# Kernel optimization log

Hardware: AMD Instinct MI355X
Metric: run time of the kernel (lower is better)

Reference implementation:

```python
import jax, jax.numpy as jnp
import numpy as np

KH, KW, STRIDE, PAD, DIL = 3, 3, 1, 1, 1


def setup_inputs() -> dict:
    key = jax.random.key(0)
    ks = jax.random.split(key, 4)
    B, C, H, W, O = 4, 256, 64, 64, 256
    K = KH * KW
    x = jax.random.normal(ks[0], (B, C, H, W), jnp.float32)
    # offset/mask conv params (original inits to zero; use small random so offsets are non-trivial)
    w_om = jax.random.normal(ks[1], (3 * K, C, KH, KW), jnp.float32) * 0.01
    b_om = jnp.zeros((3 * K,), jnp.float32)
    # main weight: kaiming_uniform_(a=1) -> gain = sqrt(2/(1+1^2)) = 1, bound = sqrt(3)/sqrt(fan_in)
    fan_in = C * K
    bound = float(np.sqrt(3.0) / np.sqrt(fan_in))
    weight = jax.random.uniform(ks[2], (O, C, KH, KW), jnp.float32, -bound, bound)
    bias = jnp.zeros((O,), jnp.float32)
    return {"x": x, "w_om": w_om, "b_om": b_om, "weight": weight, "bias": bias}


def _deform_conv2d(x, offset, mask, weight, bias):
    # torchvision.ops.deform_conv2d semantics, deformable_groups=1, stride=1, pad=1, dil=1
    B, C, H, W = x.shape
    K = KH * KW
    # torchvision offset layout: per-tap interleaved (y, x) pairs along channel dim
    off_y = offset[:, 0::2]  # [B, K, H, W]
    off_x = offset[:, 1::2]  # [B, K, H, W]
    ky = (jnp.repeat(jnp.arange(KH), KW) * DIL).astype(x.dtype)  # [K]
    kx = (jnp.tile(jnp.arange(KW), KH) * DIL).astype(x.dtype)    # [K]
    base_y = (jnp.arange(H) * STRIDE - PAD).astype(x.dtype)
    base_x = (jnp.arange(W) * STRIDE - PAD).astype(x.dtype)
    py = base_y[None, None, :, None] + ky[None, :, None, None] + off_y  # [B,K,H,W]
    px = base_x[None, None, None, :] + kx[None, :, None, None] + off_x  # [B,K,H,W]
    y0 = jnp.floor(py)
    x0 = jnp.floor(px)
    ly = py - y0
    lx = px - x0
    y0i = y0.astype(jnp.int32)
    x0i = x0.astype(jnp.int32)
    x_flat = x.reshape(B, C, H * W)

    def gather(yy, xx):
        # zero-padded gather of one bilinear corner -> [B, C, K, H, W]
        valid = ((yy >= 0) & (yy < H) & (xx >= 0) & (xx < W)).astype(x.dtype)
        idx = (jnp.clip(yy, 0, H - 1) * W + jnp.clip(xx, 0, W - 1)).reshape(B, -1)
        g = jax.vmap(lambda xf, i: jnp.take(xf, i, axis=1))(x_flat, idx)
        return g.reshape(B, C, K, H, W) * valid.reshape(B, 1, K, H, W)

    w00 = ((1 - ly) * (1 - lx))[:, None]
    w01 = ((1 - ly) * lx)[:, None]
    w10 = (ly * (1 - lx))[:, None]
    w11 = (ly * lx)[:, None]
    val = (gather(y0i, x0i) * w00 + gather(y0i, x0i + 1) * w01
           + gather(y0i + 1, x0i) * w10 + gather(y0i + 1, x0i + 1) * w11)
    cols = val * mask[:, None]  # modulated columns [B,C,K,H,W]
    out = jnp.einsum('bckhw,ock->bohw', cols, weight.reshape(weight.shape[0], C, K))
    return out + bias[None, :, None, None]


def reference(x, w_om, b_om, weight, bias):
    om = jax.lax.conv_general_dilated(
        x, w_om, (STRIDE, STRIDE), ((PAD, PAD), (PAD, PAD)),
        rhs_dilation=(DIL, DIL), dimension_numbers=('NCHW', 'OIHW', 'NCHW'),
    ) + b_om[None, :, None, None]
    K = KH * KW
    o1, o2, m = om[:, :K], om[:, K:2 * K], om[:, 2 * K:]
    offset = jnp.concatenate([o1, o2], axis=1)  # [B, 2K, H, W]
    mask = jax.nn.sigmoid(m)                    # [B, K, H, W]
    return _deform_conv2d(x, offset, mask, weight, bias)
```

## Files before the change

kernel.cpp:

```cpp
#include <hip/hip_runtime.h>
#include <stdint.h>

#define B_ 4
#define C_ 256
#define H_ 64
#define W_ 64
#define O_ 256
#define K_ 9
#define CK 2304
#define HW 4096
#define NTOT 16384

typedef __bf16 bf16x8 __attribute__((ext_vector_type(8)));
typedef __bf16 bf16x4 __attribute__((ext_vector_type(4)));
typedef float f32x4 __attribute__((ext_vector_type(4)));
typedef float f32x2 __attribute__((ext_vector_type(2)));
typedef f32x2 __attribute__((aligned(4))) f32x2u;

__device__ __forceinline__ uint16_t f2bf(float f) {
  uint32_t u = __builtin_bit_cast(uint32_t, f);
  return (uint16_t)((u + 0x7FFFu + ((u >> 16) & 1u)) >> 16);
}

__device__ __forceinline__ uint32_t pk_bf16(float a, float b) {
  uint16_t lo = __builtin_bit_cast(uint16_t, (__bf16)a);
  uint16_t hi = __builtin_bit_cast(uint16_t, (__bf16)b);
  return (uint32_t)lo | ((uint32_t)hi << 16);
}

__global__ void kA_prep(const float* __restrict__ weight, const float* __restrict__ w_om,
                        const float* __restrict__ x, uint16_t* __restrict__ wb,
                        uint16_t* __restrict__ womb, uint16_t* __restrict__ xT) {
  int bx = blockIdx.x;
  int t = threadIdx.x;
  if (bx < 256) {
    int o = bx, c = t;
    const float* wp = weight + (o * 256 + c) * 9;
#pragma unroll
    for (int k = 0; k < 9; ++k) wb[o * CK + k * 256 + c] = f2bf(wp[k]);
  } else if (bx < 283) {
    int j = bx - 256, c = t;
    const float* wp = w_om + (j * 256 + c) * 9;
#pragma unroll
    for (int k = 0; k < 9; ++k) womb[j * CK + k * 256 + c] = f2bf(wp[k]);
  } else if (bx < 288) {
    int j = 27 + (bx - 283), c = t;
#pragma unroll
    for (int k = 0; k < 9; ++k) womb[j * CK + k * 256 + c] = 0;
  } else {
    int bxl = bx - 288;
    int ct = bxl & 3;
    int hwt = (bxl >> 2) & 63;
    int b = bxl >> 8;
    int l = t & 63;
    int cq = t >> 6;

    __shared__ __align__(16) uint16_t tile[64 * 72];

    const float* xb = x + ((b * 256 + ct * 64) * HW) + hwt * 64;
#pragma unroll
    for (int i = 0; i < 16; ++i) {
      int c = cq * 16 + i;
      tile[l * 72 + c] = f2bf(xb[c * HW + l]);
    }
    __syncthreads();

    int hw = t >> 2;
    int c8 = (t & 3) * 8;
    uint16_t* dst = xT + ((size_t)b << 20) + (size_t)(hwt * 64 + hw) * 256 + ct * 64;
    *(uint4*)&dst[c8] = *(const uint4*)&tile[hw * 72 + c8];
    *(uint4*)&dst[c8 + 32] = *(const uint4*)&tile[hw * 72 + c8 + 32];
  }
}


struct GatherState {
  float wa0[4], wb0[4], wa1[4], wb1[4];
  bf16x4 r00[4], r01[4], r10[4], r11[4];
};

__device__ __forceinline__ void gather_issue(GatherState& S, const uint16_t* __restrict__ xb,
                                             const float* pypx_l,
                                             int kg, int rbase, int lane) {
#pragma unroll
  for (int j = 0; j < 4; ++j) {
    int nrow = rbase + j;
    float py = pypx_l[(0 * 9 + kg) * 64 + nrow];
    float px = pypx_l[(1 * 9 + kg) * 64 + nrow];
    float mk = pypx_l[(2 * 9 + kg) * 64 + nrow];
    float fy0 = floorf(py), fx0 = floorf(px);
    float ly = py - fy0, lx = px - fx0;
    int y0 = (int)fy0, x0 = (int)fx0;
    bool vy0 = ((unsigned)y0 < 64u), vy1 = ((unsigned)(y0 + 1) < 64u);
    bool vx0 = ((unsigned)x0 < 64u), vx1 = ((unsigned)(x0 + 1) < 64u);
    float w00 = (vy0 && vx0) ? (1.f - ly) * (1.f - lx) * mk : 0.f;
    float w01 = (vy0 && vx1) ? (1.f - ly) * lx * mk : 0.f;
    float w10 = (vy1 && vx0) ? ly * (1.f - lx) * mk : 0.f;
    float w11 = (vy1 && vx1) ? ly * lx * mk : 0.f;
    bool sel0 = (x0 >= 63);
    bool sel1 = (x0 >= 0);
    S.wa0[j] = (sel0 ? 0.f : w00) + (sel1 ? 0.f : w01);
    S.wb0[j] = (sel0 ? w00 : 0.f) + (sel1 ? w01 : 0.f);
    S.wa1[j] = (sel0 ? 0.f : w10) + (sel1 ? 0.f : w11);
    S.wb1[j] = (sel0 ? w10 : 0.f) + (sel1 ? w11 : 0.f);
    int bx0 = min(max(x0, 0), 62);
    int a0 = min(max(y0, 0), 63) * 64 + bx0;
    int a1 = min(max(y0 + 1, 0), 63) * 64 + bx0;
    S.r00[j] = *(const bf16x4*)&xb[a0 * 256 + lane * 4];
    S.r01[j] = *(const bf16x4*)&xb[a0 * 256 + 256 + lane * 4];
    S.r10[j] = *(const bf16x4*)&xb[a1 * 256 + lane * 4];
    S.r11[j] = *(const bf16x4*)&xb[a1 * 256 + 256 + lane * 4];
  }
}

__device__ __forceinline__ void gather_finish(const GatherState& S, uint16_t* bslab,
                                              int rbase, int lane) {
#pragma unroll
  for (int j = 0; j < 4; ++j) {
    int nrow = rbase + j;
    float v[4];
#pragma unroll
    for (int i = 0; i < 4; ++i)
      v[i] = S.wa0[j] * (float)S.r00[j][i] + S.wb0[j] * (float)S.r01[j][i] +
             S.wa1[j] * (float)S.r10[j][i] + S.wb1[j] * (float)S.r11[j][i];
    uint2 pk;
    pk.x = pk_bf16(v[0], v[1]);
    pk.y = pk_bf16(v[2], v[3]);
    int chunk = lane >> 1;
    int chs = (chunk & 24) | ((chunk & 7) ^ (nrow & 7));
    *(uint2*)&bslab[nrow * 256 + chs * 8 + (lane & 1) * 4] = pk;
  }
}

__device__ __forceinline__ void stageA(const uint16_t* __restrict__ wb, uint16_t* asbuf,
                                       int kbase, int t) {
#pragma unroll
  for (int i = 0; i < 4; ++i) {
    int rr = i * 64 + (t >> 3);
    const uint16_t* src = wb + rr * CK + kbase + (((t & 7) ^ (rr & 7)) << 3);
    __builtin_amdgcn_global_load_lds(
        (const __attribute__((address_space(1))) uint32_t*)src,
        (__attribute__((address_space(3))) uint32_t*)&asbuf[i * 4096 + t * 8], 16, 0, 0);
  }
}

__device__ __forceinline__ void mma_step(const uint16_t* AsP, const uint16_t* BsP,
                                         f32x4 acc[4][2], int wm, int wn, int lr, int q,
                                         int kt2) {
#pragma unroll
  for (int kc = 0; kc < 2; ++kc) {
    bf16x8 aF[4], bF[2];
#pragma unroll
    for (int i = 0; i < 4; ++i) {
      int row = wm * 64 + i * 16 + lr;
      aF[i] = *(const bf16x8*)&AsP[row * 64 + (((kc * 4 + q) ^ (row & 7)) << 3)];
    }
#pragma unroll
    for (int j = 0; j < 2; ++j) {
      int row = wn * 32 + j * 16 + lr;
      int kidx = kt2 * 8 + kc * 4 + q;
      int chs = (kidx & 24) | ((kidx & 7) ^ (row & 7));
      bF[j] = *(const bf16x8*)&BsP[row * 256 + chs * 8];
    }
#pragma unroll
    for (int i = 0; i < 4; ++i)
#pragma unroll
      for (int j = 0; j < 2; ++j)
        acc[i][j] = __builtin_amdgcn_mfma_f32_16x16x32_bf16(aF[i], bF[j], acc[i][j], 0, 0, 0);
  }
}

__global__ __launch_bounds__(512, 2) void k123(const uint16_t* __restrict__ wb,
                                               const uint16_t* __restrict__ womb,
                                               const uint16_t* __restrict__ xT,
                                               const float* __restrict__ b_om,
                                               const float* __restrict__ bias,
                                               float* __restrict__ out) {
  __shared__ __align__(16) uint16_t As[2][16384];
  __shared__ __align__(16) uint16_t Bs[16384];
  __shared__ float pypx_l[3 * 9 * 64];

  int t = threadIdx.x;
  int lane = t & 63;
  int wid = __builtin_amdgcn_readfirstlane(t >> 6);
  int lr = lane & 15, q = lane >> 4;
  int bx = blockIdx.x;
  int swz = (bx & 7) * 32 + (bx >> 3);
  int n0 = swz * 64;
  int b = n0 >> 12;
  int hw0 = n0 & 4095;
  const uint16_t* xb = xT + ((size_t)b << 20);

  {
    uint16_t* Apro = As[0];
    int jh = wid >> 2, ng = wid & 3;
    const uint16_t* zrow = womb + 31 * CK;
    f32x4 accp = {0.f, 0.f, 0.f, 0.f};

    for (int k = 0; k < 9; ++k) {
      int dy = k / 3 - 1, dx = k - (k / 3) * 3 - 1;
#pragma unroll
      for (int i = 0; i < 2; ++i) {
        int id = i * 512 + t;
        int row = id >> 5, c5 = id & 31;
        int cs = (c5 & 24) | ((c5 & 7) ^ (row & 7));
        const uint16_t* src = womb + row * CK + k * 256 + cs * 8;
        __builtin_amdgcn_global_load_lds(
            (const __attribute__((address_space(1))) uint32_t*)src,
            (__attribute__((address_space(3))) uint32_t*)&Apro[row * 256 + c5 * 8], 16, 0, 0);
      }
#pragma unroll
      for (int i = 0; i < 4; ++i) {
        int id = i * 512 + t;
        int nrow = id >> 5, c5 = id & 31;
        int hw = (n0 + nrow) & 4095;
        int y = hw >> 6, xx = hw & 63;
        int ny = y + dy, nx = xx + dx;
        bool valid = ((unsigned)ny < 64u) && ((unsigned)nx < 64u);
        int row_g = (ny << 6) + nx;
        int cs = (c5 & 24) | ((c5 & 7) ^ (nrow & 7));
        const uint16_t* src = valid ? (xb + row_g * 256 + cs * 8) : (zrow + cs * 8);
        __builtin_amdgcn_global_load_lds(
            (const __attribute__((address_space(1))) uint32_t*)src,
            (__attribute__((address_space(3))) uint32_t*)&Bs[nrow * 256 + c5 * 8], 16, 0, 0);
      }
      __syncthreads();
#pragma unroll
      for (int kt = 0; kt < 8; ++kt) {
        int kidx = kt * 4 + q;
        int arow = jh * 16 + lr;
        int achs = (kidx & 24) | ((kidx & 7) ^ (arow & 7));
        bf16x8 aF = *(const bf16x8*)&Apro[arow * 256 + achs * 8];
        int brow = ng * 16 + lr;
        int bchs = (kidx & 24) | ((kidx & 7) ^ (brow & 7));
        bf16x8 bF = *(const bf16x8*)&Bs[brow * 256 + bchs * 8];
        accp = __builtin_amdgcn_mfma_f32_16x16x32_bf16(aF, bF, accp, 0, 0, 0);
      }
      __syncthreads();
    }

    int nn = ng * 16 + lr;
    int hwp = (n0 + nn) & 4095;
    int yp = hwp >> 6, xp = hwp & 63;
#pragma unroll
    for (int r = 0; r < 4; ++r) {
      int j = jh * 16 + q * 4 + r;
      if (j < 27) {
        float v = accp[r] + b_om[j];
        if (j < 18) {
          int k = j >> 1;
          if ((j & 1) == 0)
            pypx_l[(0 * 9 + k) * 64 + nn] = (float)(yp - 1 + k / 3) + v;
          else
            pypx_l[(1 * 9 + k) * 64 + nn] = (float)(xp - 1 + k % 3) + v;
        } else {
          pypx_l[(2 * 9 + (j - 18)) * 64 + nn] = 1.f / (1.f + __expf(-v));
        }
      }
    }
    __syncthreads();
  }

  f32x4 acc[4][2];
  const f32x4 zero = {0.f, 0.f, 0.f, 0.f};
#pragma unroll
  for (int i = 0; i < 4; ++i)
#pragma unroll
    for (int j = 0; j < 2; ++j) acc[i][j] = zero;

  int wm = wid >> 1, wn = wid & 1;
  GatherState S;
  int wrow = wid * 8;

  gather_issue(S, xb, pypx_l, 0, wrow, lane);
  gather_finish(S, Bs, wrow, lane);
  gather_issue(S, xb, pypx_l, 0, wrow + 4, lane);
  gather_finish(S, Bs, wrow + 4, lane);
  stageA(wb, As[0], 0, t);
  __syncthreads();

  for (int k = 0; k < 9; ++k) {
    for (int kt2 = 0; kt2 < 4; ++kt2) {
      if (!(k == 8 && kt2 == 3)) {
        int kb2 = (kt2 == 3) ? (k + 1) * 256 : k * 256 + (kt2 + 1) * 64;
        stageA(wb, As[(kt2 + 1) & 1], kb2, t);
      }
      mma_step(As[kt2 & 1], Bs, acc, wm, wn, lr, q, kt2);
      __syncthreads();
    }
    if (k < 8) {
      gather_issue(S, xb, pypx_l, k + 1, wrow, lane);
      gather_finish(S, Bs, wrow, lane);
      gather_issue(S, xb, pypx_l, k + 1, wrow + 4, lane);
      gather_finish(S, Bs, wrow + 4, lane);
      __syncthreads();
    }
  }

#pragma unroll
  for (int i = 0; i < 4; ++i) {
#pragma unroll
    for (int r = 0; r < 4; ++r) {
      int o = wm * 64 + i * 16 + q * 4 + r;
      float bv = bias[o];
      float* orow = out + (b * O_ + o) * HW + hw0;
#pragma unroll
      for (int j = 0; j < 2; ++j) orow[wn * 32 + j * 16 + lr] = acc[i][j][r] + bv;
    }
  }
}

__global__ void k0_wconv(const float* __restrict__ weight, uint16_t* __restrict__ wb) {
  int idx = blockIdx.x * 256 + threadIdx.x;
  if (idx >= O_ * CK) return;
  int o = idx / CK;
  int rem = idx - o * CK;
  int k = rem >> 8;
  int c = rem & 255;
  wb[idx] = f2bf(weight[(o * C_ + c) * K_ + k]);
}

__global__ void k1_offconv(const float* __restrict__ x, const float* __restrict__ w_om,
                           const float* __restrict__ b_om, float* __restrict__ pypxmk) {
  int bx = blockIdx.x;
  int jq = bx % 7;
  int h = (bx / 7) % H_;
  int b = bx / (7 * H_);
  int t = threadIdx.x;
  int w = t & 63;
  int cs = __builtin_amdgcn_readfirstlane(t >> 6);

  float acc[4] = {0.f, 0.f, 0.f, 0.f};
  const float* xb = x + (b * C_) * HW;

  for (int ci = 0; ci < 64; ++ci) {
    int c = cs * 64 + ci;
    const float* xr = xb + c * HW;
    float xv[3][3];
#pragma unroll
    for (int r = 0; r < 3; ++r) {
      int y = h - 1 + r;
      bool yv = ((unsigned)y < 64u);
#pragma unroll
      for (int dx = 0; dx < 3; ++dx) {
        int xx = w - 1 + dx;
        bool v = yv && ((unsigned)xx < 64u);
        xv[r][dx] = v ? xr[y * 64 + xx] : 0.f;
      }
    }
    const float* wp = w_om + ((jq * 4) * C_ + c) * 9;
#pragma unroll
    for (int jj = 0; jj < 4; ++jj) {
      int j = jq * 4 + jj;
      int jeff = (j < 27) ? jj : 0;
      const float* wj = wp + jeff * (C_ * 9);
      float a = 0.f;
#pragma unroll
      for (int r = 0; r < 3; ++r)
#pragma unroll
        for (int dx = 0; dx < 3; ++dx)
          a = fmaf(xv[r][dx], wj[r * 3 + dx], a);
      acc[jj] += a;
    }
  }

  __shared__ float red[4][4][64];
#pragma unroll
  for (int jj = 0; jj < 4; ++jj) red[cs][jj][w] = acc[jj];
  __syncthreads();

  int jj = t >> 6;
  int j = jq * 4 + jj;
  if (j < 27) {
    float s = red[0][jj][w] + red[1][jj][w] + red[2][jj][w] + red[3][jj][w] + b_om[j];
    float* pyA = pypxmk;
    float* pxA = pypxmk + 147456;
    float* mkA = pypxmk + 294912;
    if (j < 18) {
      int k = j >> 1;
      int off = (b * 9 + k) * HW + h * 64 + w;
      if ((j & 1) == 0)
        pyA[off] = (float)(h - 1 + k / 3) + s;
      else
        pxA[off] = (float)(w - 1 + k % 3) + s;
    } else {
      int k = j - 18;
      mkA[(b * 9 + k) * HW + h * 64 + w] = 1.f / (1.f + __expf(-s));
    }
  }
}

__global__ void k2_fb(const float* __restrict__ x, const float* __restrict__ pypxmk,
                      uint16_t* __restrict__ cols) {
  int bx = blockIdx.x;
  int cg2 = bx & 15;
  int h = (bx >> 4) & 63;
  int b = bx >> 10;
  int t = threadIdx.x;
  int w = t & 63;
  int g = t >> 6;

  const float* pyA = pypxmk;
  const float* pxA = pypxmk + 147456;
  const float* mkA = pypxmk + 294912;

  __shared__ uint16_t tile[64 * 146];
  const float* xb = x + b * C_ * HW;
  int cbase = cg2 * 16 + g * 4;

#pragma unroll
  for (int k = 0; k < 9; ++k) {
    int poff = (b * 9 + k) * HW + h * 64 + w;
    float py = pyA[poff];
    float px = pxA[poff];
    float mk = mkA[poff];
    float fy0 = floorf(py), fx0 = floorf(px);
    float ly = py - fy0, lx = px - fx0;
    int y0 = (int)fy0, x0 = (int)fx0;
    bool vy0 = ((unsigned)y0 < 64u), vy1 = ((unsigned)(y0 + 1) < 64u);
    bool vx0 = ((unsigned)x0 < 64u), vx1 = ((unsigned)(x0 + 1) < 64u);
    float w00 = (vy0 && vx0) ? (1.f - ly) * (1.f - lx) * mk : 0.f;
    float w01 = (vy0 && vx1) ? (1.f - ly) * lx * mk : 0.f;
    float w10 = (vy1 && vx0) ? ly * (1.f - lx) * mk : 0.f;
    float w11 = (vy1 && vx1) ? ly * lx * mk : 0.f;
    bool sel0 = (x0 >= 63);
    bool sel1 = (x0 >= 0);
    float wa0 = (sel0 ? 0.f : w00) + (sel1 ? 0.f : w01);
    float wb0 = (sel0 ? w00 : 0.f) + (sel1 ? w01 : 0.f);
    float wa1 = (sel0 ? 0.f : w10) + (sel1 ? 0.f : w11);
    float wb1 = (sel0 ? w10 : 0.f) + (sel1 ? w11 : 0.f);
    int bx0 = min(max(x0, 0), 62);
    int a0 = min(max(y0, 0), 63) * 64 + bx0;
    int a1 = min(max(y0 + 1, 0), 63) * 64 + bx0;

#pragma unroll
    for (int cp = 0; cp < 2; ++cp) {
      const float* xcA = xb + (cbase + cp * 2) * HW;
      const float* xcB = xcA + HW;
      f32x2 A0 = *(const f32x2u*)&xcA[a0];
      f32x2 A1 = *(const f32x2u*)&xcA[a1];
      f32x2 B0 = *(const f32x2u*)&xcB[a0];
      f32x2 B1 = *(const f32x2u*)&xcB[a1];
      float rA = wa0 * A0.x + wb0 * A0.y + wa1 * A1.x + wb1 * A1.y;
      float rB = wa0 * B0.x + wb0 * B0.y + wa1 * B1.x + wb1 * B1.y;
      *(uint32_t*)&tile[w * 146 + k * 16 + g * 4 + cp * 2] = pk_bf16(rA, rB);
    }
  }
  __syncthreads();

#pragma unroll
  for (int it = 0; it < 18; ++it) {
    int u = t + it * 256;
    int wu = u / 72;
    int rem = u - wu * 72;
    int k = rem >> 3;
    int cd = rem & 7;
    uint32_t val = *(const uint32_t*)&tile[wu * 146 + rem * 2];
    int n = b * HW + h * 64 + wu;
    int dst = n * CK + k * 256 + cg2 * 16 + cd * 2;
    *(uint32_t*)&cols[dst] = val;
  }
}

__global__ void k3_flex(const uint16_t* __restrict__ wb, const uint16_t* __restrict__ cols,
                        const float* __restrict__ bias, float* __restrict__ out) {
  int bx = blockIdx.x;
  int mt = bx & 1;
  int nt = bx >> 1;
  int o0 = mt * 128;
  int n0 = nt * 128;
  int t = threadIdx.x;
  int lane = t & 63;
  int wid = t >> 6;
  int wm = wid >> 1, wn = wid & 1;
  int lr = lane & 15, q = lane >> 4;

  __shared__ __align__(16) uint16_t As[128 * 32];
  __shared__ __align__(16) uint16_t Bs[128 * 32];

  f32x4 acc[4][4];
  const f32x4 zero = {0.f, 0.f, 0.f, 0.f};
#pragma unroll
  for (int i = 0; i < 4; ++i)
#pragma unroll
    for (int j = 0; j < 4; ++j) acc[i][j] = zero;

  int r0 = t >> 2;
  int koff = (t & 3) * 8;
  const uint16_t* gA = wb + (o0 + r0) * CK + koff;
  const uint16_t* gB = cols + (n0 + r0) * CK + koff;

  for (int kt = 0; kt < 72; ++kt) {
    int k0 = kt * 32;
    __builtin_amdgcn_global_load_lds(
        (const __attribute__((address_space(1))) uint32_t*)(gA + k0),
        (__attribute__((address_space(3))) uint32_t*)&As[t * 8], 16, 0, 0);
    __builtin_amdgcn_global_load_lds(
        (const __attribute__((address_space(1))) uint32_t*)(gA + 64 * CK + k0),
        (__attribute__((address_space(3))) uint32_t*)&As[2048 + t * 8], 16, 0, 0);
    __builtin_amdgcn_global_load_lds(
        (const __attribute__((address_space(1))) uint32_t*)(gB + k0),
        (__attribute__((address_space(3))) uint32_t*)&Bs[t * 8], 16, 0, 0);
    __builtin_amdgcn_global_load_lds(
        (const __attribute__((address_space(1))) uint32_t*)(gB + 64 * CK + k0),
        (__attribute__((address_space(3))) uint32_t*)&Bs[2048 + t * 8], 16, 0, 0);
    __syncthreads();

    bf16x8 aF[4], bF[4];
#pragma unroll
    for (int i = 0; i < 4; ++i)
      aF[i] = *(const bf16x8*)&As[(wm * 64 + i * 16 + lr) * 32 + q * 8];
#pragma unroll
    for (int j = 0; j < 4; ++j)
      bF[j] = *(const bf16x8*)&Bs[(wn * 64 + j * 16 + lr) * 32 + q * 8];
#pragma unroll
    for (int i = 0; i < 4; ++i)
#pragma unroll
      for (int j = 0; j < 4; ++j)
        acc[i][j] = __builtin_amdgcn_mfma_f32_16x16x32_bf16(aF[i], bF[j], acc[i][j], 0, 0, 0);
    __syncthreads();
  }

  int bb = n0 >> 12;
  int hw0 = n0 & 4095;
#pragma unroll
  for (int i = 0; i < 4; ++i) {
#pragma unroll
    for (int r = 0; r < 4; ++r) {
      int o = o0 + wm * 64 + i * 16 + q * 4 + r;
      float bv = bias[o];
      float* orow = out + (bb * O_ + o) * HW + hw0;
#pragma unroll
      for (int j = 0; j < 4; ++j) orow[wn * 64 + j * 16 + lr] = acc[i][j][r] + bv;
    }
  }
}

extern "C" void kernel_launch(void* const* d_in, const int* in_sizes, int n_in,
                              void* d_out, int out_size, void* d_ws, size_t ws_size,
                              hipStream_t stream) {
  const float* x = (const float*)d_in[0];
  const float* w_om = (const float*)d_in[1];
  const float* b_om = (const float*)d_in[2];
  const float* weight = (const float*)d_in[3];
  const float* bias = (const float*)d_in[4];
  float* out = (float*)d_out;

  char* ws = (char*)d_ws;
  uint16_t* wb = (uint16_t*)ws;
  uint16_t* womb = (uint16_t*)(ws + 1179648);
  uint16_t* xT = (uint16_t*)(ws + 1327104);

  if (ws_size >= 11485184ull) {
    hipLaunchKernelGGL(kA_prep, dim3(1312), dim3(256), 0, stream, weight, w_om, x, wb, womb, xT);
    hipLaunchKernelGGL(k123, dim3(256), dim3(512), 0, stream, wb, womb, xT, b_om, bias, out);
  } else {
    float* pypx_fb = (float*)(ws + 1179648);
    uint16_t* colsf = (uint16_t*)(ws + 2949120);
    hipLaunchKernelGGL(k0_wconv, dim3(2304), dim3(256), 0, stream, weight, wb);
    hipLaunchKernelGGL(k1_offconv, dim3(4 * 64 * 7), dim3(256), 0, stream, x, w_om, b_om, pypx_fb);
    hipLaunchKernelGGL(k2_fb, dim3(4 * 64 * 16), dim3(256), 0, stream, x, pypx_fb, colsf);
    hipLaunchKernelGGL(k3_flex, dim3(256), dim3(256), 0, stream, wb, colsf, bias, out);
  }
}
```

Before: 147.3 us.

## Halve pixel tile per block to 32 and launch twice as many blocks

The fused deformable-conv kernel now handles 32 output pixels per block instead of 64 and launches 512 blocks instead of 256. The main GEMM A-tile staging and MMA step are rewritten for a 32-wide K chunk with a new swizzle. The offset-conv prologue splits the channel reduction across two warp halves and combines them through shared memory. The goal is more parallelism and occupancy on 256 CUs by shrinking shared memory and raising launch bounds to 4 blocks per CU. In exchange, each weight tile is reused across fewer pixels, and there are more barriers per unit of work.

```diff
diff --git a/kernel.cpp b/kernel.cpp
--- a/kernel.cpp
+++ b/kernel.cpp
@@ -74,6 +74,8 @@
 }
 
 
+#define NT 32
+
 struct GatherState {
   float wa0[4], wb0[4], wa1[4], wb1[4];
   bf16x4 r00[4], r01[4], r10[4], r11[4];
@@ -85,9 +87,9 @@
 #pragma unroll
   for (int j = 0; j < 4; ++j) {
     int nrow = rbase + j;
-    float py = pypx_l[(0 * 9 + kg) * 64 + nrow];
-    float px = pypx_l[(1 * 9 + kg) * 64 + nrow];
-    float mk = pypx_l[(2 * 9 + kg) * 64 + nrow];
+    float py = pypx_l[(0 * 9 + kg) * NT + nrow];
+    float px = pypx_l[(1 * 9 + kg) * NT + nrow];
+    float mk = pypx_l[(2 * 9 + kg) * NT + nrow];
     float fy0 = floorf(py), fx0 = floorf(px);
     float ly = py - fy0, lx = px - fx0;
     int y0 = (int)fy0, x0 = (int)fx0;
@@ -132,68 +134,67 @@
   }
 }
 
-__device__ __forceinline__ void stageA(const uint16_t* __restrict__ wb, uint16_t* asbuf,
-                                       int kbase, int t) {
-#pragma unroll
-  for (int i = 0; i < 4; ++i) {
-    int rr = i * 64 + (t >> 3);
-    const uint16_t* src = wb + rr * CK + kbase + (((t & 7) ^ (rr & 7)) << 3);
+__device__ __forceinline__ void stageA32(const uint16_t* __restrict__ wb, uint16_t* asbuf,
+                                         int kbase, int t) {
+#pragma unroll
+  for (int i = 0; i < 2; ++i) {
+    int slot = i * 512 + t;
+    int row = slot >> 2, p = slot & 3;
+    const uint16_t* src = wb + row * CK + kbase + ((p ^ ((row >> 1) & 3)) << 3);
     __builtin_amdgcn_global_load_lds(
         (const __attribute__((address_space(1))) uint32_t*)src,
-        (__attribute__((address_space(3))) uint32_t*)&asbuf[i * 4096 + t * 8], 16, 0, 0);
-  }
-}
-
-__device__ __forceinline__ void mma_step(const uint16_t* AsP, const uint16_t* BsP,
-                                         f32x4 acc[4][2], int wm, int wn, int lr, int q,
-                                         int kt2) {
-#pragma unroll
-  for (int kc = 0; kc < 2; ++kc) {
-    bf16x8 aF[4], bF[2];
-#pragma unroll
-    for (int i = 0; i < 4; ++i) {
-      int row = wm * 64 + i * 16 + lr;
-      aF[i] = *(const bf16x8*)&AsP[row * 64 + (((kc * 4 + q) ^ (row & 7)) << 3)];
-    }
-#pragma unroll
-    for (int j = 0; j < 2; ++j) {
-      int row = wn * 32 + j * 16 + lr;
-      int kidx = kt2 * 8 + kc * 4 + q;
-      int chs = (kidx & 24) | ((kidx & 7) ^ (row & 7));
-      bF[j] = *(const bf16x8*)&BsP[row * 256 + chs * 8];
-    }
-#pragma unroll
-    for (int i = 0; i < 4; ++i)
-#pragma unroll
-      for (int j = 0; j < 2; ++j)
-        acc[i][j] = __builtin_amdgcn_mfma_f32_16x16x32_bf16(aF[i], bF[j], acc[i][j], 0, 0, 0);
-  }
-}
-
-__global__ __launch_bounds__(512, 2) void k123(const uint16_t* __restrict__ wb,
+        (__attribute__((address_space(3))) uint32_t*)&asbuf[row * 32 + p * 8], 16, 0, 0);
+  }
+}
+
+__device__ __forceinline__ void mma32(const uint16_t* AsP, const uint16_t* BsP,
+                                      f32x4 acc[2][2], int wm, int lr, int q, int s) {
+  bf16x8 aF[2], bF[2];
+#pragma unroll
+  for (int i = 0; i < 2; ++i) {
+    int arow = wm * 32 + i * 16 + lr;
+    aF[i] = *(const bf16x8*)&AsP[arow * 32 + ((q ^ ((arow >> 1) & 3)) << 3)];
+  }
+#pragma unroll
+  for (int j = 0; j < 2; ++j) {
+    int brow = j * 16 + lr;
+    int kidx = s * 4 + q;
+    int chs = (kidx & 24) | ((kidx & 7) ^ (brow & 7));
+    bF[j] = *(const bf16x8*)&BsP[brow * 256 + chs * 8];
+  }
+#pragma unroll
+  for (int i = 0; i < 2; ++i)
+#pragma unroll
+    for (int j = 0; j < 2; ++j)
+      acc[i][j] = __builtin_amdgcn_mfma_f32_16x16x32_bf16(aF[i], bF[j], acc[i][j], 0, 0, 0);
+}
+
+__global__ __launch_bounds__(512, 4) void k123(const uint16_t* __restrict__ wb,
                                                const uint16_t* __restrict__ womb,
                                                const uint16_t* __restrict__ xT,
                                                const float* __restrict__ b_om,
                                                const float* __restrict__ bias,
                                                float* __restrict__ out) {
-  __shared__ __align__(16) uint16_t As[2][16384];
-  __shared__ __align__(16) uint16_t Bs[16384];
-  __shared__ float pypx_l[3 * 9 * 64];
+  __shared__ __align__(16) uint16_t As[2][8192];
+  __shared__ __align__(16) uint16_t Bs[8192];
+  __shared__ float pypx_l[3 * 9 * NT];
 
   int t = threadIdx.x;
   int lane = t & 63;
   int wid = __builtin_amdgcn_readfirstlane(t >> 6);
   int lr = lane & 15, q = lane >> 4;
   int bx = blockIdx.x;
-  int swz = (bx & 7) * 32 + (bx >> 3);
-  int n0 = swz * 64;
+  int swz = (bx & 7) * 64 + (bx >> 3);
+  int n0 = swz * NT;
   int b = n0 >> 12;
   int hw0 = n0 & 4095;
   const uint16_t* xb = xT + ((size_t)b << 20);
 
   {
-    uint16_t* Apro = As[0];
-    int jh = wid >> 2, ng = wid & 3;
+    uint16_t* Apro = (uint16_t*)As;
+    int ch = wid >> 2;
+    int jh = (wid >> 1) & 1;
+    int nh = wid & 1;
     const uint16_t* zrow = womb + 31 * CK;
     f32x4 accp = {0.f, 0.f, 0.f, 0.f};
 
@@ -201,8 +202,8 @@
       int dy = k / 3 - 1, dx = k - (k / 3) * 3 - 1;
 #pragma unroll
       for (int i = 0; i < 2; ++i) {
-        int id = i * 512 + t;
-        int row = id >> 5, c5 = id & 31;
+        int slot = i * 512 + t;
+        int row = slot >> 5, c5 = slot & 31;
         int cs = (c5 & 24) | ((c5 & 7) ^ (row & 7));
         const uint16_t* src = womb + row * CK + k * 256 + cs * 8;
         __builtin_amdgcn_global_load_lds(
@@ -210,9 +211,9 @@
             (__attribute__((address_space(3))) uint32_t*)&Apro[row * 256 + c5 * 8], 16, 0, 0);
       }
 #pragma unroll
-      for (int i = 0; i < 4; ++i) {
-        int id = i * 512 + t;
-        int nrow = id >> 5, c5 = id & 31;
+      for (int i = 0; i < 2; ++i) {
+        int slot = i * 512 + t;
+        int nrow = slot >> 5, c5 = slot & 31;
         int hw = (n0 + nrow) & 4095;
         int y = hw >> 6, xx = hw & 63;
         int ny = y + dy, nx = xx + dx;
@@ -226,12 +227,12 @@
       }
       __syncthreads();
 #pragma unroll
-      for (int kt = 0; kt < 8; ++kt) {
-        int kidx = kt * 4 + q;
+      for (int kt = 0; kt < 4; ++kt) {
+        int kidx = ch * 16 + kt * 4 + q;
         int arow = jh * 16 + lr;
         int achs = (kidx & 24) | ((kidx & 7) ^ (arow & 7));
         bf16x8 aF = *(const bf16x8*)&Apro[arow * 256 + achs * 8];
-        int brow = ng * 16 + lr;
+        int brow = nh * 16 + lr;
         int bchs = (kidx & 24) | ((kidx & 7) ^ (brow & 7));
         bf16x8 bF = *(const bf16x8*)&Bs[brow * 256 + bchs * 8];
         accp = __builtin_amdgcn_mfma_f32_16x16x32_bf16(aF, bF, accp, 0, 0, 0);
@@ -239,73 +240,78 @@
       __syncthreads();
     }
 
-    int nn = ng * 16 + lr;
-    int hwp = (n0 + nn) & 4095;
-    int yp = hwp >> 6, xp = hwp & 63;
-#pragma unroll
-    for (int r = 0; r < 4; ++r) {
-      int j = jh * 16 + q * 4 + r;
-      if (j < 27) {
-        float v = accp[r] + b_om[j];
-        if (j < 18) {
-          int k = j >> 1;
-          if ((j & 1) == 0)
-            pypx_l[(0 * 9 + k) * 64 + nn] = (float)(yp - 1 + k / 3) + v;
-          else
-            pypx_l[(1 * 9 + k) * 64 + nn] = (float)(xp - 1 + k % 3) + v;
-        } else {
-          pypx_l[(2 * 9 + (j - 18)) * 64 + nn] = 1.f / (1.f + __expf(-v));
+    float* red = (float*)As;
+    int rbase = ((jh * 2 + nh) * 64 + lane) * 4;
+    if (ch == 1) {
+#pragma unroll
+      for (int r = 0; r < 4; ++r) red[rbase + r] = accp[r];
+    }
+    __syncthreads();
+    if (ch == 0) {
+      int nn = nh * 16 + lr;
+      int hwp = (n0 + nn) & 4095;
+      int yp = hwp >> 6, xp = hwp & 63;
+#pragma unroll
+      for (int r = 0; r < 4; ++r) {
+        int j = jh * 16 + q * 4 + r;
+        if (j < 27) {
+          float v = accp[r] + red[rbase + r] + b_om[j];
+          if (j < 18) {
+            int k = j >> 1;
+            if ((j & 1) == 0)
+              pypx_l[(0 * 9 + k) * NT + nn] = (float)(yp - 1 + k / 3) + v;
+            else
+              pypx_l[(1 * 9 + k) * NT + nn] = (float)(xp - 1 + k % 3) + v;
+          } else {
+            pypx_l[(2 * 9 + (j - 18)) * NT + nn] = 1.f / (1.f + __expf(-v));
+          }
         }
       }
     }
     __syncthreads();
   }
 
-  f32x4 acc[4][2];
+  f32x4 acc[2][2];
   const f32x4 zero = {0.f, 0.f, 0.f, 0.f};
 #pragma unroll
-  for (int i = 0; i < 4; ++i)
+  for (int i = 0; i < 2; ++i)
 #pragma unroll
     for (int j = 0; j < 2; ++j) acc[i][j] = zero;
 
-  int wm = wid >> 1, wn = wid & 1;
+  int wm = wid;
   GatherState S;
-  int wrow = wid * 8;
+  int wrow = wid * 4;
 
   gather_issue(S, xb, pypx_l, 0, wrow, lane);
   gather_finish(S, Bs, wrow, lane);
-  gather_issue(S, xb, pypx_l, 0, wrow + 4, lane);
-  gather_finish(S, Bs, wrow + 4, lane);
-  stageA(wb, As[0], 0, t);
+  stageA32(wb, As[0], 0, t);
   __syncthreads();
 
   for (int k = 0; k < 9; ++k) {
-    for (int kt2 = 0; kt2 < 4; ++kt2) {
-      if (!(k == 8 && kt2 == 3)) {
-        int kb2 = (kt2 == 3) ? (k + 1) * 256 : k * 256 + (kt2 + 1) * 64;
-        stageA(wb, As[(kt2 + 1) & 1], kb2, t);
+    for (int s = 0; s < 8; ++s) {
+      if (!(k == 8 && s == 7)) {
+        int kb = (s == 7) ? (k + 1) * 256 : k * 256 + (s + 1) * 32;
+        stageA32(wb, As[(s + 1) & 1], kb, t);
       }
-      mma_step(As[kt2 & 1], Bs, acc, wm, wn, lr, q, kt2);
+      mma32(As[s & 1], Bs, acc, wm, lr, q, s);
       __syncthreads();
     }
     if (k < 8) {
       gather_issue(S, xb, pypx_l, k + 1, wrow, lane);
       gather_finish(S, Bs, wrow, lane);
-      gather_issue(S, xb, pypx_l, k + 1, wrow + 4, lane);
-      gather_finish(S, Bs, wrow + 4, lane);
       __syncthreads();
     }
   }
 
 #pragma unroll
-  for (int i = 0; i < 4; ++i) {
+  for (int i = 0; i < 2; ++i) {
 #pragma unroll
     for (int r = 0; r < 4; ++r) {
-      int o = wm * 64 + i * 16 + q * 4 + r;
+      int o = wm * 32 + i * 16 + q * 4 + r;
       float bv = bias[o];
       float* orow = out + (b * O_ + o) * HW + hw0;
 #pragma unroll
-      for (int j = 0; j < 2; ++j) orow[wn * 32 + j * 16 + lr] = acc[i][j][r] + bv;
+      for (int j = 0; j < 2; ++j) orow[j * 16 + lr] = acc[i][j][r] + bv;
     }
   }
 }
@@ -553,7 +559,7 @@
 
   if (ws_size >= 11485184ull) {
     hipLaunchKernelGGL(kA_prep, dim3(1312), dim3(256), 0, stream, weight, w_om, x, wb, womb, xT);
-    hipLaunchKernelGGL(k123, dim3(256), dim3(512), 0, stream, wb, womb, xT, b_om, bias, out);
+    hipLaunchKernelGGL(k123, dim3(512), dim3(512), 0, stream, wb, womb, xT, b_om, bias, out);
   } else {
     float* pypx_fb = (float*)(ws + 1179648);
     uint16_t* colsf = (uint16_t*)(ws + 2949120);
```

After: 149.2 us. No clear change (+1.3%).

## Stage weight tiles in 128-wide K chunks and overlap A load with gather

Applied to the files above, without the earlier changes.

Replaces the double-buffered 64-wide weight staging (four MMA steps per tap, each with its own barrier) with a single 128-wide buffer loaded twice per tap. The next tap's first A chunk is issued alongside the deformable gather so the two overlap, and there are fewer barriers per tap. In exchange, the second half-chunk load of each tap is no longer overlapped with MMA work and sits between two barriers, which could expose global-load latency.

```diff
diff --git a/kernel.cpp b/kernel.cpp
--- a/kernel.cpp
+++ b/kernel.cpp
@@ -132,33 +132,38 @@
   }
 }
 
-__device__ __forceinline__ void stageA(const uint16_t* __restrict__ wb, uint16_t* asbuf,
-                                       int kbase, int t) {
-#pragma unroll
-  for (int i = 0; i < 4; ++i) {
-    int rr = i * 64 + (t >> 3);
-    const uint16_t* src = wb + rr * CK + kbase + (((t & 7) ^ (rr & 7)) << 3);
+__device__ __forceinline__ void stageA128(const uint16_t* __restrict__ wb, uint16_t* asbuf,
+                                          int kbase, int t) {
+#pragma unroll
+  for (int i = 0; i < 8; ++i) {
+    int slot = i * 512 + t;
+    int row = slot >> 4;
+    int ch = slot & 15;
+    int sc = (ch & 8) | ((ch & 7) ^ (row & 7));
+    const uint16_t* src = wb + row * CK + kbase + sc * 8;
     __builtin_amdgcn_global_load_lds(
         (const __attribute__((address_space(1))) uint32_t*)src,
-        (__attribute__((address_space(3))) uint32_t*)&asbuf[i * 4096 + t * 8], 16, 0, 0);
-  }
-}
-
-__device__ __forceinline__ void mma_step(const uint16_t* AsP, const uint16_t* BsP,
-                                         f32x4 acc[4][2], int wm, int wn, int lr, int q,
-                                         int kt2) {
-#pragma unroll
-  for (int kc = 0; kc < 2; ++kc) {
+        (__attribute__((address_space(3))) uint32_t*)&asbuf[row * 128 + ch * 8], 16, 0, 0);
+  }
+}
+
+__device__ __forceinline__ void mma128(const uint16_t* AsP, const uint16_t* BsP,
+                                       f32x4 acc[4][2], int wm, int wn, int lr, int q,
+                                       int khalf) {
+#pragma unroll
+  for (int kc = 0; kc < 4; ++kc) {
     bf16x8 aF[4], bF[2];
 #pragma unroll
     for (int i = 0; i < 4; ++i) {
       int row = wm * 64 + i * 16 + lr;
-      aF[i] = *(const bf16x8*)&AsP[row * 64 + (((kc * 4 + q) ^ (row & 7)) << 3)];
+      int ka = kc * 4 + q;
+      int sch = (ka & 8) | ((ka & 7) ^ (row & 7));
+      aF[i] = *(const bf16x8*)&AsP[row * 128 + sch * 8];
     }
 #pragma unroll
     for (int j = 0; j < 2; ++j) {
       int row = wn * 32 + j * 16 + lr;
-      int kidx = kt2 * 8 + kc * 4 + q;
+      int kidx = khalf * 16 + kc * 4 + q;
       int chs = (kidx & 24) | ((kidx & 7) ^ (row & 7));
       bF[j] = *(const bf16x8*)&BsP[row * 256 + chs * 8];
     }
@@ -176,7 +181,7 @@
                                                const float* __restrict__ b_om,
                                                const float* __restrict__ bias,
                                                float* __restrict__ out) {
-  __shared__ __align__(16) uint16_t As[2][16384];
+  __shared__ __align__(16) uint16_t As[32768];
   __shared__ __align__(16) uint16_t Bs[16384];
   __shared__ float pypx_l[3 * 9 * 64];
 
@@ -192,7 +197,7 @@
   const uint16_t* xb = xT + ((size_t)b << 20);
 
   {
-    uint16_t* Apro = As[0];
+    uint16_t* Apro = As;
     int jh = wid >> 2, ng = wid & 3;
     const uint16_t* zrow = womb + 31 * CK;
     f32x4 accp = {0.f, 0.f, 0.f, 0.f};
@@ -276,23 +281,22 @@
   gather_finish(S, Bs, wrow, lane);
   gather_issue(S, xb, pypx_l, 0, wrow + 4, lane);
   gather_finish(S, Bs, wrow + 4, lane);
-  stageA(wb, As[0], 0, t);
+  stageA128(wb, As, 0, t);
   __syncthreads();
 
   for (int k = 0; k < 9; ++k) {
-    for (int kt2 = 0; kt2 < 4; ++kt2) {
-      if (!(k == 8 && kt2 == 3)) {
-        int kb2 = (kt2 == 3) ? (k + 1) * 256 : k * 256 + (kt2 + 1) * 64;
-        stageA(wb, As[(kt2 + 1) & 1], kb2, t);
-      }
-      mma_step(As[kt2 & 1], Bs, acc, wm, wn, lr, q, kt2);
-      __syncthreads();
-    }
+    mma128(As, Bs, acc, wm, wn, lr, q, 0);
+    __syncthreads();
+    stageA128(wb, As, k * 256 + 128, t);
+    __syncthreads();
+    mma128(As, Bs, acc, wm, wn, lr, q, 1);
+    __syncthreads();
     if (k < 8) {
       gather_issue(S, xb, pypx_l, k + 1, wrow, lane);
       gather_finish(S, Bs, wrow, lane);
       gather_issue(S, xb, pypx_l, k + 1, wrow + 4, lane);
       gather_finish(S, Bs, wrow + 4, lane);
+      stageA128(wb, As, (k + 1) * 256, t);
       __syncthreads();
     }
   }
```

New measurement: 149.5 us. About the same (+1.4%).
